# Optimization experiments

Measured on AMD Instinct MI355X. Metric: run time of the kernel, lower is better.

Reference implementation:

```python
import math
import jax, jax.numpy as jnp
import numpy as np

B, L, D_MODEL, N_HEADS = 4, 4096, 1024, 16
HEAD_DIM = D_MODEL // N_HEADS
NUM_LANDMARKS = 128


def setup_inputs() -> dict:
    key = jax.random.key(0)
    ks = jax.random.split(key, 7)
    s = 1.0 / math.sqrt(D_MODEL)
    return {
        "x": jax.random.normal(ks[0], (B, L, D_MODEL), dtype=jnp.float32),
        "Wq": jax.random.uniform(ks[1], (D_MODEL, D_MODEL), jnp.float32, -s, s),
        "bq": jax.random.uniform(ks[2], (D_MODEL,), jnp.float32, -s, s),
        "Wk": jax.random.uniform(ks[3], (D_MODEL, D_MODEL), jnp.float32, -s, s),
        "bk": jax.random.uniform(ks[4], (D_MODEL,), jnp.float32, -s, s),
        "Wv": jax.random.uniform(ks[5], (D_MODEL, D_MODEL), jnp.float32, -s, s),
        "bv": jax.random.uniform(ks[6], (D_MODEL,), jnp.float32, -s, s),
    }


def _split_heads(t):
    b, l, _ = t.shape
    return t.reshape(b, l, N_HEADS, HEAD_DIM).transpose(0, 2, 1, 3)  # [b,h,l,d]


def _iterative_inv(mat, n_iter=6):
    # Newton-Schulz pseudo-inverse on [b,h,m,m]; 'original' init uses global max.
    I = jnp.eye(mat.shape[-1], dtype=mat.dtype)
    K = mat
    V = K.swapaxes(-1, -2) / jnp.max(jnp.sum(K, axis=-2))
    for _ in range(n_iter):
        KV = jnp.matmul(K, V)
        V = jnp.matmul(0.25 * V, 13.0 * I - jnp.matmul(KV, 15.0 * I - jnp.matmul(KV, 7.0 * I - KV)))
    return V


def reference(x, Wq, bq, Wk, bk, Wv, bv):
    Q = _split_heads(x @ Wq.T + bq)
    K = _split_heads(x @ Wk.T + bk)
    V = _split_heads(x @ Wv.T + bv)
    b, h, l, d = Q.shape
    # mask is internally all-ones (module overwrites any passed mask), so the
    # -1e9*(1-mask) bias term is identically zero and mask-multiplies are no-ops.
    scale = 1.0 / math.sqrt(math.sqrt(HEAD_DIM))
    Q = Q * scale
    K = K * scale
    seg = l // NUM_LANDMARKS
    Q_lm = Q.reshape(b, h, NUM_LANDMARKS, seg, d).mean(axis=-2)  # [b,h,m,d]
    K_lm = K.reshape(b, h, NUM_LANDMARKS, seg, d).mean(axis=-2)
    kernel_1 = jax.nn.softmax(jnp.einsum('bhld,bhmd->bhlm', Q, K_lm), axis=-1)   # [b,h,l,m]
    kernel_2 = jax.nn.softmax(jnp.einsum('bhmd,bhnd->bhmn', Q_lm, K_lm), axis=-1)  # [b,h,m,m]
    kernel_3 = jax.nn.softmax(jnp.einsum('bhmd,bhld->bhml', Q_lm, K), axis=-1)   # [b,h,m,l]
    X = jnp.matmul(jnp.matmul(kernel_1, _iterative_inv(kernel_2)), jnp.matmul(kernel_3, V))  # [b,h,l,d]
    out = X.transpose(0, 2, 1, 3).reshape(b, l, h * d)
    return out
```

## Files before the change

kernel.cpp:

```cpp
#include <hip/hip_runtime.h>
#include <hip/hip_bf16.h>
#include <stdint.h>

#define DEV __device__ __forceinline__

typedef __attribute__((ext_vector_type(8))) short bf16x8;
typedef __attribute__((ext_vector_type(4))) short short4v;
typedef __attribute__((ext_vector_type(4))) float f32x4;

static constexpr int LL = 4096;
static constexpr int NH = 16;
static constexpr int HD = 64;
static constexpr int DM = 1024;
static constexpr int NL = 128;
static constexpr int BH = 64;
static constexpr int NSPLIT = 16;
static constexpr float QK_SCALE = 0.35355339059327379f;

DEV short f2bf(float f) {
  union { __hip_bfloat16 h; short s; } u;
  u.h = __float2bfloat16(f);
  return u.s;
}
DEV float bf2f(unsigned short s) {
  union { unsigned u; float f; } u;
  u.u = ((unsigned)s) << 16;
  return u.f;
}
DEV float clampf(float v) {
  return fminf(fmaxf(v, -1e6f), 1e6f);
}

DEV f32x4 mfma16(bf16x8 a, bf16x8 b, f32x4 c) {
  return __builtin_amdgcn_mfma_f32_16x16x32_bf16(a, b, c, 0, 0, 0);
}

DEV void gl2lds16(const void* g, void* l) {
  __builtin_amdgcn_global_load_lds(
      (const __attribute__((address_space(1))) void*)g,
      (__attribute__((address_space(3))) void*)l, 16, 0, 0);
}

DEV void split1(float f, short& hi, short& lo) {
  unsigned u = __float_as_uint(f);
  hi = (short)(u >> 16);
  lo = f2bf(f - __uint_as_float(u & 0xffff0000u));
}

DEV void split8(const float* av, bf16x8& hv, bf16x8& lv) {
#pragma unroll
  for (int e = 0; e < 8; e++) {
    short hi, lo;
    split1(av[e], hi, lo);
    hv[e] = hi;
    lv[e] = lo;
  }
}

__global__ __launch_bounds__(256) void cvt_kernel(
    const void* __restrict__ xv,
    const void* __restrict__ Wq, const void* __restrict__ Wk, const void* __restrict__ Wv,
    const void* __restrict__ bq, const void* __restrict__ bk, const void* __restrict__ bv,
    unsigned short* __restrict__ xb, unsigned short* __restrict__ Wb,
    float* __restrict__ bb)
{
  const int bid = blockIdx.x, t = threadIdx.x;
  __shared__ int cnt;

  auto probe_f32 = [&](const unsigned short* p) -> int {
    if (t == 0) cnt = 0;
    __syncthreads();
    int c = 0;
    for (int i = t; i < 512; i += 256) {
      unsigned e = (p[2 * i] >> 7) & 0xFF;
      if (e > 90 && e < 160) c++;
    }
    atomicAdd(&cnt, c);
    __syncthreads();
    int r = (cnt < 358);
    __syncthreads();
    return r;
  };

  auto cvt8 = [&](const void* src, unsigned short* dst, size_t i, int f32) {
    if (f32) {
      const float* s = (const float*)src + i * 8;
      f32x4 a = *(const f32x4*)s;
      f32x4 b = *(const f32x4*)(s + 4);
      bf16x8 o;
      o[0] = f2bf(a[0]); o[1] = f2bf(a[1]); o[2] = f2bf(a[2]); o[3] = f2bf(a[3]);
      o[4] = f2bf(b[0]); o[5] = f2bf(b[1]); o[6] = f2bf(b[2]); o[7] = f2bf(b[3]);
      *(bf16x8*)(dst + i * 8) = o;
    } else {
      *(bf16x8*)(dst + i * 8) =
          *(const bf16x8*)((const unsigned short*)src + i * 8);
    }
  };

  if (bid < 1536) {
    const int q = bid / 512;
    const void* src = (q == 0) ? Wq : ((q == 1) ? Wk : Wv);
    const int f32 = probe_f32((const unsigned short*)src);
    const size_t i = (size_t)(bid % 512) * 256 + t;
    cvt8(src, Wb + (size_t)q * DM * DM, i, f32);
  } else if (bid == 1536) {
    for (int q = 0; q < 3; q++) {
      const void* src = (q == 0) ? bq : ((q == 1) ? bk : bv);
      const int f32 = probe_f32((const unsigned short*)src);
      for (int i = t; i < DM; i += 256)
        bb[q * DM + i] = f32 ? ((const float*)src)[i]
                             : bf2f(((const unsigned short*)src)[i]);
      __syncthreads();
    }
  } else {
    const int xi = bid - 1537;
    const int f32 = probe_f32((const unsigned short*)xv);
#pragma unroll
    for (int k = 0; k < 4; k++) {
      const size_t i = (size_t)xi * 1024 + k * 256 + t;
      cvt8(xv, xb, i, f32);
    }
  }
}

__global__ __launch_bounds__(256, 2) void proj_kernel(
    const unsigned short* __restrict__ xb,
    const unsigned short* __restrict__ Wb,
    const float* __restrict__ bb,
    unsigned short* __restrict__ Qo, unsigned short* __restrict__ Ko,
    unsigned short* __restrict__ Vo,
    float* __restrict__ Qlm, float* __restrict__ Klm,
    unsigned short* __restrict__ Qlmb, unsigned short* __restrict__ Klmb)
{
  __shared__ __align__(16) short As[2][128 * 32];
  __shared__ __align__(16) short Bs[2][128 * 32];

  const int t = threadIdx.x;
  const int w = t >> 6;
  const int l = t & 63;
  const int lane16 = l & 15, lgrp = l >> 4;

  const int bid = blockIdx.x;
  const int mt = bid & 127;
  const int nt = bid >> 7;
  const int which = nt >> 3;
  const int m0 = mt * 128;
  const int ncol0 = (nt & 7) * 128;

  unsigned short* outp = (which == 0) ? Qo : ((which == 1) ? Ko : Vo);
  const float scl = (which == 2) ? 1.0f : QK_SCALE;

  const int srow = w * 16 + (l >> 2);
  const int skc = (l & 3) * 8;
  const unsigned short* gA = xb + (size_t)(m0 + srow) * DM + skc;
  const unsigned short* gB = Wb + (size_t)which * DM * DM + (size_t)(ncol0 + srow) * DM + skc;
  short* lA0 = As[0] + w * 512;
  short* lA1 = As[1] + w * 512;
  short* lB0 = Bs[0] + w * 512;
  short* lB1 = Bs[1] + w * 512;

  const int wm = (w >> 1) * 64;
  const int wn = (w & 1) * 64;

  f32x4 acc[4][4];
#pragma unroll
  for (int i = 0; i < 4; i++)
#pragma unroll
    for (int j = 0; j < 4; j++) acc[i][j] = f32x4{0.f, 0.f, 0.f, 0.f};

  for (int kk = 0; kk < DM; kk += 64) {
    gl2lds16(gA + kk, lA0);
    gl2lds16(gA + kk + 64 * DM, lA0 + 2048);
    gl2lds16(gA + kk + 32, lA1);
    gl2lds16(gA + kk + 32 + 64 * DM, lA1 + 2048);
    gl2lds16(gB + kk, lB0);
    gl2lds16(gB + kk + 64 * DM, lB0 + 2048);
    gl2lds16(gB + kk + 32, lB1);
    gl2lds16(gB + kk + 32 + 64 * DM, lB1 + 2048);
    __syncthreads();
#pragma unroll
    for (int kc = 0; kc < 2; kc++) {
      bf16x8 af[4], bfv[4];
#pragma unroll
      for (int i = 0; i < 4; i++) {
        af[i]  = *(const bf16x8*)&As[kc][(wm + i * 16 + lane16) * 32 + lgrp * 8];
        bfv[i] = *(const bf16x8*)&Bs[kc][(wn + i * 16 + lane16) * 32 + lgrp * 8];
      }
#pragma unroll
      for (int i = 0; i < 4; i++)
#pragma unroll
        for (int j = 0; j < 4; j++)
          acc[i][j] = mfma16(af[i], bfv[j], acc[i][j]);
    }
    __syncthreads();
  }

  const int b = m0 >> 12;
  const int hh = (ncol0 + wn) >> 6;
  float bv4[4];
#pragma unroll
  for (int j = 0; j < 4; j++)
    bv4[j] = bb[which * DM + ncol0 + wn + j * 16 + lane16];

  float seg[2][4];
#pragma unroll
  for (int s = 0; s < 2; s++)
#pragma unroll
    for (int j = 0; j < 4; j++) seg[s][j] = 0.f;

#pragma unroll
  for (int i = 0; i < 4; i++) {
#pragma unroll
    for (int j = 0; j < 4; j++) {
#pragma unroll
      for (int r = 0; r < 4; r++) {
        float v = (acc[i][j][r] + bv4[j]) * scl;
        int row = wm + i * 16 + lgrp * 4 + r;
        int li = (m0 + row) & 4095;
        int dd = (wn + j * 16 + lane16) & 63;
        outp[(((size_t)(b * NH + hh)) * LL + li) * HD + dd] = (unsigned short)f2bf(v);
        seg[i >> 1][j] += v;
      }
    }
  }
  if (which < 2) {
    float* lmb = (which == 0) ? Qlm : Klm;
    unsigned short* lmbb = (which == 0) ? Qlmb : Klmb;
#pragma unroll
    for (int s = 0; s < 2; s++) {
#pragma unroll
      for (int j = 0; j < 4; j++) {
        float ssum = seg[s][j];
        ssum += __shfl_xor(ssum, 16, 64);
        ssum += __shfl_xor(ssum, 32, 64);
        if (lgrp == 0) {
          int m = ((m0 + wm + s * 32) & 4095) >> 5;
          int dd = (wn + j * 16 + lane16) & 63;
          float mv = clampf(ssum * (1.0f / 32.0f));
          size_t idx = (((size_t)(b * NH + hh)) * NL + m) * HD + dd;
          lmb[idx] = mv;
          lmbb[idx] = (unsigned short)f2bf(mv);
        }
      }
    }
  }
}

__global__ __launch_bounds__(256, 1) void mid_kernel(
    const unsigned short* __restrict__ Qlmb, const unsigned short* __restrict__ K,
    const unsigned short* __restrict__ V,
    float* __restrict__ op, float* __restrict__ mp, float* __restrict__ lp,
    const float* __restrict__ Qlm, const float* __restrict__ Klm,
    float* __restrict__ k2, float* __restrict__ colsum_g)
{
  constexpr int LT = 64;
  constexpr int ST = 72;
  __shared__ __align__(16) short q_s[NL * ST];
  __shared__ __align__(16) short k_s[LT * ST];
  __shared__ __align__(16) short vt_s[HD * ST];
  __shared__ __align__(16) short p_s[NL * ST];

  const int t = threadIdx.x;

  if (blockIdx.x < BH * NSPLIT) {
    const int bid = blockIdx.x;
    const int bh = bid >> 4;
    const int sp = bid & (NSPLIT - 1);
    const int w = t >> 6, l = t & 63;
    const int lane16 = l & 15, lgrp = l >> 4;
    const int wm = w * 32;
    const unsigned short* Kp = K + (size_t)bh * LL * HD;
    const unsigned short* Vp = V + (size_t)bh * LL * HD;

    for (int i = t; i < NL * HD / 4; i += 256) {
      int flat = i * 4, rr = flat >> 6, dd = flat & 63;
      *(uint2*)&q_s[rr * ST + dd] = *(const uint2*)&Qlmb[(size_t)bh * NL * HD + flat];
    }

    f32x4 oacc[2][4];
    float mrun[2][4], lrun[2][4];
#pragma unroll
    for (int i = 0; i < 2; i++)
#pragma unroll
      for (int j = 0; j < 4; j++) oacc[i][j] = f32x4{0.f, 0.f, 0.f, 0.f};
#pragma unroll
    for (int i = 0; i < 2; i++)
#pragma unroll
      for (int r = 0; r < 4; r++) { mrun[i][r] = -3.0e38f; lrun[i][r] = 0.f; }

    constexpr int TPS = LL / LT / NSPLIT;
    for (int lt = sp * TPS; lt < (sp + 1) * TPS; lt++) {
      const int l0 = lt * LT;
      for (int i = t; i < LT * HD / 4; i += 256) {
        int flat = i * 4, rr = flat >> 6, dd = flat & 63;
        *(uint2*)&k_s[rr * ST + dd] = *(const uint2*)&Kp[(size_t)(l0 + rr) * HD + dd];
        uint2 raw = *(const uint2*)&Vp[(size_t)(l0 + rr) * HD + dd];
        vt_s[(dd + 0) * ST + rr] = (short)(raw.x & 0xffff);
        vt_s[(dd + 1) * ST + rr] = (short)(raw.x >> 16);
        vt_s[(dd + 2) * ST + rr] = (short)(raw.y & 0xffff);
        vt_s[(dd + 3) * ST + rr] = (short)(raw.y >> 16);
      }
      __syncthreads();

      f32x4 sacc[2][4];
#pragma unroll
      for (int i = 0; i < 2; i++)
#pragma unroll
        for (int j = 0; j < 4; j++) sacc[i][j] = f32x4{0.f, 0.f, 0.f, 0.f};
#pragma unroll
      for (int kc = 0; kc < 2; kc++) {
        bf16x8 aq[2];
#pragma unroll
        for (int i = 0; i < 2; i++)
          aq[i] = *(const bf16x8*)&q_s[(wm + i * 16 + lane16) * ST + kc * 32 + lgrp * 8];
#pragma unroll
        for (int j = 0; j < 4; j++) {
          bf16x8 bk = *(const bf16x8*)&k_s[(j * 16 + lane16) * ST + kc * 32 + lgrp * 8];
#pragma unroll
          for (int i = 0; i < 2; i++) sacc[i][j] = mfma16(aq[i], bk, sacc[i][j]);
        }
      }

#pragma unroll
      for (int i = 0; i < 2; i++) {
#pragma unroll
        for (int r = 0; r < 4; r++) {
          float tm = fmaxf(fmaxf(sacc[i][0][r], sacc[i][1][r]),
                           fmaxf(sacc[i][2][r], sacc[i][3][r]));
          tm = fmaxf(tm, __shfl_xor(tm, 1, 16));
          tm = fmaxf(tm, __shfl_xor(tm, 2, 16));
          tm = fmaxf(tm, __shfl_xor(tm, 4, 16));
          tm = fmaxf(tm, __shfl_xor(tm, 8, 16));
          float mnew = fmaxf(mrun[i][r], tm);
          float al = __expf(mrun[i][r] - mnew);
          float rs = 0.f;
#pragma unroll
          for (int j = 0; j < 4; j++) {
            float e = __expf(sacc[i][j][r] - mnew);
            sacc[i][j][r] = e;
            rs += e;
          }
          rs += __shfl_xor(rs, 1, 16);
          rs += __shfl_xor(rs, 2, 16);
          rs += __shfl_xor(rs, 4, 16);
          rs += __shfl_xor(rs, 8, 16);
          lrun[i][r] = lrun[i][r] * al + rs;
          mrun[i][r] = mnew;
#pragma unroll
          for (int j = 0; j < 4; j++) oacc[i][j][r] *= al;
          int row = wm + i * 16 + lgrp * 4 + r;
#pragma unroll
          for (int j = 0; j < 4; j++)
            p_s[row * ST + j * 16 + lane16] = f2bf(sacc[i][j][r]);
        }
      }
      __syncthreads();

#pragma unroll
      for (int kc = 0; kc < 2; kc++) {
        bf16x8 ap[2];
#pragma unroll
        for (int i = 0; i < 2; i++)
          ap[i] = *(const bf16x8*)&p_s[(wm + i * 16 + lane16) * ST + kc * 32 + lgrp * 8];
#pragma unroll
        for (int j = 0; j < 4; j++) {
          bf16x8 bv = *(const bf16x8*)&vt_s[(j * 16 + lane16) * ST + kc * 32 + lgrp * 8];
#pragma unroll
          for (int i = 0; i < 2; i++) oacc[i][j] = mfma16(ap[i], bv, oacc[i][j]);
        }
      }
      __syncthreads();
    }

    float* opp = op + ((size_t)(bh * NSPLIT + sp)) * NL * HD;
#pragma unroll
    for (int i = 0; i < 2; i++)
#pragma unroll
      for (int j = 0; j < 4; j++)
#pragma unroll
        for (int r = 0; r < 4; r++) {
          int row = wm + i * 16 + lgrp * 4 + r;
          int dd = j * 16 + lane16;
          opp[(size_t)row * HD + dd] = oacc[i][j][r];
        }
    if (lane16 == 0) {
      const size_t base = (size_t)(bh * NSPLIT + sp) * NL;
#pragma unroll
      for (int i = 0; i < 2; i++)
#pragma unroll
        for (int r = 0; r < 4; r++) {
          int row = wm + i * 16 + lgrp * 4 + r;
          mp[base + row] = mrun[i][r];
          lp[base + row] = lrun[i][r];
        }
    }
  } else {
    float* cs = (float*)q_s;
    const int bid = blockIdx.x - BH * NSPLIT;
    const int bh = bid >> 3;
    const int rc = bid & 7;
    const int r = t >> 4;
    const int c = t & 15;
    const int row = rc * 16 + r;
    const float* Q = Qlm + ((size_t)bh * NL + row) * HD;
    const float* Kf = Klm + (size_t)bh * NL * HD;
    float* k2p = k2 + (size_t)bh * NL * NL;

    for (int i = t; i < NL; i += 256) cs[i] = 0.f;

    f32x4 q4[16];
#pragma unroll
    for (int d = 0; d < 16; d++) q4[d] = *(const f32x4*)&Q[d * 4];

    float dots[8];
#pragma unroll
    for (int g = 0; g < 8; g++) {
      const float* kr = Kf + (size_t)(c + g * 16) * HD;
      float s = 0.f;
#pragma unroll
      for (int d = 0; d < 16; d++) {
        f32x4 k4 = *(const f32x4*)&kr[d * 4];
        s += q4[d][0] * k4[0];
        s += q4[d][1] * k4[1];
        s += q4[d][2] * k4[2];
        s += q4[d][3] * k4[3];
      }
      dots[g] = s;
    }

    float mx = dots[0];
#pragma unroll
    for (int g = 1; g < 8; g++) mx = fmaxf(mx, dots[g]);
    mx = fmaxf(mx, __shfl_xor(mx, 1, 16));
    mx = fmaxf(mx, __shfl_xor(mx, 2, 16));
    mx = fmaxf(mx, __shfl_xor(mx, 4, 16));
    mx = fmaxf(mx, __shfl_xor(mx, 8, 16));

    float sum = 0.f;
#pragma unroll
    for (int g = 0; g < 8; g++) {
      float e = __expf(dots[g] - mx);
      dots[g] = e;
      sum += e;
    }
    sum += __shfl_xor(sum, 1, 16);
    sum += __shfl_xor(sum, 2, 16);
    sum += __shfl_xor(sum, 4, 16);
    sum += __shfl_xor(sum, 8, 16);
    const float inv = 1.0f / fmaxf(sum, 1e-30f);

    __syncthreads();
#pragma unroll
    for (int g = 0; g < 8; g++) {
      float p = dots[g] * inv;
      k2p[(size_t)row * NL + c + g * 16] = p;
      atomicAdd(&cs[c + g * 16], p);
    }
    __syncthreads();
    for (int i = t; i < NL; i += 256) atomicAdd(&colsum_g[bh * NL + i], cs[i]);
  }
}

__global__ __launch_bounds__(256) void k3v_combine(
    const float* __restrict__ op, const float* __restrict__ mp,
    const float* __restrict__ lp, float* __restrict__ k3v)
{
  const int idx = blockIdx.x * 256 + threadIdx.x;
  const int dd = idx & 63;
  const int row = (idx >> 6) & 127;
  const int bh = idx >> 13;
  (void)dd;
  float m = -3.0e38f;
  float ms[NSPLIT];
#pragma unroll
  for (int s = 0; s < NSPLIT; s++) {
    ms[s] = mp[(size_t)(bh * NSPLIT + s) * NL + row];
    m = fmaxf(m, ms[s]);
  }
  float o = 0.f, ltot = 0.f;
#pragma unroll
  for (int s = 0; s < NSPLIT; s++) {
    float sc = __expf(ms[s] - m);
    ltot += lp[(size_t)(bh * NSPLIT + s) * NL + row] * sc;
    o += op[((size_t)(bh * NSPLIT + s) * NL + row) * HD + dd] * sc;
  }
  k3v[idx] = clampf(o / fmaxf(ltot, 1e-30f));
}

__global__ __launch_bounds__(512, 1) void ns_kernel(
    const float* __restrict__ k2, const float* __restrict__ colsum_g,
    const float* __restrict__ k3v, unsigned short* __restrict__ w2t)
{
  constexpr int VST = 132;
  constexpr int BST = 136;
  __shared__ __align__(16) float Vf[NL * VST];
  __shared__ __align__(16) short Bth[NL * BST];
  __shared__ __align__(16) short Btl[NL * BST];
  __shared__ float wmx[8];
  __shared__ float amax_s;

  const int bh = blockIdx.x, t = threadIdx.x;
  const int w = t >> 6, l = t & 63;
  const int lane16 = l & 15, lgrp = l >> 4;
  const float* K2 = k2 + (size_t)bh * NL * NL;

  float am = 0.f;
  for (int i = t; i < BH * NL; i += 512) am = fmaxf(am, colsum_g[i]);
#pragma unroll
  for (int o = 1; o < 64; o <<= 1) am = fmaxf(am, __shfl_xor(am, o, 64));
  if (l == 0) wmx[w] = am;
  __syncthreads();
  if (t == 0) {
    float m = wmx[0];
#pragma unroll
    for (int i = 1; i < 8; i++) m = fmaxf(m, wmx[i]);
    amax_s = m;
  }
  __syncthreads();
  const float inva = 1.0f / fmaxf(amax_s, 1e-30f);

  bf16x8 k2hi[4], k2lo[4];
#pragma unroll
  for (int kk = 0; kk < 4; kk++) {
    const float* ap = K2 + (size_t)(w * 16 + lane16) * NL + kk * 32 + lgrp * 8;
    f32x4 a0 = *(const f32x4*)ap;
    f32x4 a1 = *(const f32x4*)(ap + 4);
    float av[8] = {a0[0], a0[1], a0[2], a0[3], a1[0], a1[1], a1[2], a1[3]};
    split8(av, k2hi[kk], k2lo[kk]);
  }

  for (int i = t; i < NL * NL; i += 512) {
    int rr = i >> 7, cc = i & 127;
    float v = clampf(K2[(size_t)cc * NL + rr] * inva);
    Vf[rr * VST + cc] = v;
    short hi, lo; split1(v, hi, lo);
    Bth[cc * BST + rr] = hi;
    Btl[cc * BST + rr] = lo;
  }
  __syncthreads();

  f32x4 macc[8], vacc[8];

  auto mmA = [&](const bf16x8* ahi, const bf16x8* alo) {
#pragma unroll
    for (int j = 0; j < 8; j++) macc[j] = f32x4{0.f, 0.f, 0.f, 0.f};
#pragma unroll
    for (int kk = 0; kk < 4; kk++) {
#pragma unroll
      for (int j = 0; j < 8; j++) {
        const int bo = (j * 16 + lane16) * BST + kk * 32 + lgrp * 8;
        bf16x8 bh_ = *(const bf16x8*)&Bth[bo];
        bf16x8 bl_ = *(const bf16x8*)&Btl[bo];
        macc[j] = mfma16(alo[kk], bh_, macc[j]);
        macc[j] = mfma16(ahi[kk], bl_, macc[j]);
        macc[j] = mfma16(ahi[kk], bh_, macc[j]);
      }
    }
  };

  auto mmV = [&]() {
    bf16x8 ahi[4], alo[4];
#pragma unroll
    for (int kk = 0; kk < 4; kk++) {
      const float* ap = &Vf[(w * 16 + lane16) * VST + kk * 32 + lgrp * 8];
      f32x4 a0 = *(const f32x4*)ap;
      f32x4 a1 = *(const f32x4*)(ap + 4);
      float av[8] = {a0[0], a0[1], a0[2], a0[3], a1[0], a1[1], a1[2], a1[3]};
      split8(av, ahi[kk], alo[kk]);
    }
    mmA(ahi, alo);
  };

  auto writeBt = [&]() {
#pragma unroll
    for (int j = 0; j < 8; j++) {
      short4v hv, lv;
#pragma unroll
      for (int r = 0; r < 4; r++) {
        float c = clampf(macc[j][r]);
        short hi, lo; split1(c, hi, lo);
        hv[r] = hi; lv[r] = lo;
      }
      const int base = (j * 16 + lane16) * BST + w * 16 + lgrp * 4;
      *(short4v*)&Bth[base] = hv;
      *(short4v*)&Btl[base] = lv;
    }
  };

  for (int it = 0; it < 6; it++) {
    mmA(k2hi, k2lo);
    __syncthreads();
    writeBt();
    __syncthreads();

    mmV();
#pragma unroll
    for (int j = 0; j < 8; j++)
#pragma unroll
      for (int r = 0; r < 4; r++)
        vacc[j][r] = 3.25f * Vf[(w * 16 + lgrp * 4 + r) * VST + j * 16 + lane16]
                   - 3.75f * macc[j][r];
    __syncthreads();
#pragma unroll
    for (int j = 0; j < 8; j++)
#pragma unroll
      for (int r = 0; r < 4; r++)
        Vf[(w * 16 + lgrp * 4 + r) * VST + j * 16 + lane16] = clampf(macc[j][r]);
    __syncthreads();

    mmV();
#pragma unroll
    for (int j = 0; j < 8; j++)
#pragma unroll
      for (int r = 0; r < 4; r++) vacc[j][r] += 1.75f * macc[j][r];
    __syncthreads();
#pragma unroll
    for (int j = 0; j < 8; j++)
#pragma unroll
      for (int r = 0; r < 4; r++)
        Vf[(w * 16 + lgrp * 4 + r) * VST + j * 16 + lane16] = clampf(macc[j][r]);
    __syncthreads();

    mmV();
    __syncthreads();
#pragma unroll
    for (int j = 0; j < 8; j++) {
      short4v hv, lv;
#pragma unroll
      for (int r = 0; r < 4; r++) {
        float v = clampf(vacc[j][r] - 0.25f * macc[j][r]);
        Vf[(w * 16 + lgrp * 4 + r) * VST + j * 16 + lane16] = v;
        short hi, lo; split1(v, hi, lo);
        hv[r] = hi; lv[r] = lo;
      }
      const int base = (j * 16 + lane16) * BST + w * 16 + lgrp * 4;
      *(short4v*)&Bth[base] = hv;
      *(short4v*)&Btl[base] = lv;
    }
    __syncthreads();
  }

  const float* kvp = k3v + (size_t)bh * NL * HD;
  for (int i = t; i < NL * HD; i += 512) {
    int rr = i >> 6, dd = i & 63;
    float f = kvp[i];
    short hi, lo; split1(f, hi, lo);
    Bth[dd * BST + rr] = hi;
    Btl[dd * BST + rr] = lo;
  }
  __syncthreads();

  const int wr = (w & 3);
  const int wc = (w >> 2);
  f32x4 oacc[4];
#pragma unroll
  for (int j = 0; j < 4; j++) oacc[j] = f32x4{0.f, 0.f, 0.f, 0.f};
#pragma unroll
  for (int kk = 0; kk < 4; kk++) {
    const int ao = (wr * 16 + lane16) * BST + kk * 32 + lgrp * 8;
    bf16x8 ahi = *(const bf16x8*)&Bth[ao];
    bf16x8 alo = *(const bf16x8*)&Btl[ao];
#pragma unroll
    for (int j = 0; j < 4; j++) {
      const float* bp = &Vf[((wc * 4 + j) * 16 + lane16) * VST + kk * 32 + lgrp * 8];
      f32x4 b0 = *(const f32x4*)bp;
      f32x4 b1 = *(const f32x4*)(bp + 4);
      float bvv[8] = {b0[0], b0[1], b0[2], b0[3], b1[0], b1[1], b1[2], b1[3]};
      bf16x8 bhv, blv;
      split8(bvv, bhv, blv);
      oacc[j] = mfma16(alo, bhv, oacc[j]);
      oacc[j] = mfma16(ahi, blv, oacc[j]);
      oacc[j] = mfma16(ahi, bhv, oacc[j]);
    }
  }
  unsigned short* outp = w2t + (size_t)bh * HD * NL;
#pragma unroll
  for (int j = 0; j < 4; j++)
#pragma unroll
    for (int r = 0; r < 4; r++) {
      int dd = wr * 16 + lgrp * 4 + r;
      int m  = (wc * 4 + j) * 16 + lane16;
      outp[(size_t)dd * NL + m] = (unsigned short)f2bf(clampf(oacc[j][r]));
    }
}

__global__ __launch_bounds__(256, 2) void final_kernel(
    const unsigned short* __restrict__ Q, const unsigned short* __restrict__ Klmb,
    const unsigned short* __restrict__ w2t, float* __restrict__ outp)
{
  constexpr int KSD = 72;
  constexpr int PSD = 136;
  __shared__ __align__(16) short klm_s[NL * KSD];
  __shared__ __align__(16) short p_s[NL * PSD];

  const int bid = blockIdx.x;
  const int bh = bid >> 5, lt = bid & 31;
  const int l0 = lt * NL;
  const int t = threadIdx.x, w = t >> 6, l = t & 63;
  const int lane16 = l & 15, lgrp = l >> 4;
  const int wm = w * 32;
  const unsigned short* Qp = Q + (size_t)bh * LL * HD;
  const unsigned short* Kp = Klmb + (size_t)bh * NL * HD;
  const unsigned short* Wp = w2t + (size_t)bh * HD * NL;

  for (int i = t; i < NL * HD / 4; i += 256) {
    int flat = i * 4, rr = flat >> 6, dd = flat & 63;
    *(uint2*)&klm_s[rr * KSD + dd] = *(const uint2*)&Kp[flat];
  }
  __syncthreads();

  f32x4 sacc[2][8];
#pragma unroll
  for (int i = 0; i < 2; i++)
#pragma unroll
    for (int j = 0; j < 8; j++) sacc[i][j] = f32x4{0.f, 0.f, 0.f, 0.f};
#pragma unroll
  for (int kc = 0; kc < 2; kc++) {
    bf16x8 aq[2];
#pragma unroll
    for (int i = 0; i < 2; i++)
      aq[i] = *(const bf16x8*)&Qp[(size_t)(l0 + wm + i * 16 + lane16) * HD + kc * 32 + lgrp * 8];
#pragma unroll
    for (int j = 0; j < 8; j++) {
      bf16x8 bk = *(const bf16x8*)&klm_s[(j * 16 + lane16) * KSD + kc * 32 + lgrp * 8];
#pragma unroll
      for (int i = 0; i < 2; i++) sacc[i][j] = mfma16(aq[i], bk, sacc[i][j]);
    }
  }

#pragma unroll
  for (int i = 0; i < 2; i++) {
#pragma unroll
    for (int r = 0; r < 4; r++) {
      float mx = -1e30f;
#pragma unroll
      for (int j = 0; j < 8; j++) mx = fmaxf(mx, sacc[i][j][r]);
      mx = fmaxf(mx, __shfl_xor(mx, 1, 16));
      mx = fmaxf(mx, __shfl_xor(mx, 2, 16));
      mx = fmaxf(mx, __shfl_xor(mx, 4, 16));
      mx = fmaxf(mx, __shfl_xor(mx, 8, 16));
      float sum = 0.f;
#pragma unroll
      for (int j = 0; j < 8; j++) {
        float e = __expf(sacc[i][j][r] - mx);
        sacc[i][j][r] = e;
        sum += e;
      }
      sum += __shfl_xor(sum, 1, 16);
      sum += __shfl_xor(sum, 2, 16);
      sum += __shfl_xor(sum, 4, 16);
      sum += __shfl_xor(sum, 8, 16);
      float inv = 1.0f / fmaxf(sum, 1e-30f);
      int row = wm + i * 16 + lgrp * 4 + r;
#pragma unroll
      for (int j = 0; j < 8; j++)
        p_s[row * PSD + j * 16 + lane16] = f2bf(sacc[i][j][r] * inv);
    }
  }
  __syncthreads();

  f32x4 oacc[2][4];
#pragma unroll
  for (int i = 0; i < 2; i++)
#pragma unroll
    for (int j = 0; j < 4; j++) oacc[i][j] = f32x4{0.f, 0.f, 0.f, 0.f};
#pragma unroll
  for (int kc = 0; kc < 4; kc++) {
    bf16x8 ap[2];
#pragma unroll
    for (int i = 0; i < 2; i++)
      ap[i] = *(const bf16x8*)&p_s[(wm + i * 16 + lane16) * PSD + kc * 32 + lgrp * 8];
#pragma unroll
    for (int j = 0; j < 4; j++) {
      bf16x8 bw = *(const bf16x8*)&Wp[(size_t)(j * 16 + lane16) * NL + kc * 32 + lgrp * 8];
#pragma unroll
      for (int i = 0; i < 2; i++) oacc[i][j] = mfma16(ap[i], bw, oacc[i][j]);
    }
  }

  const int b = bh >> 4, h = bh & 15;
#pragma unroll
  for (int i = 0; i < 2; i++)
#pragma unroll
    for (int j = 0; j < 4; j++)
#pragma unroll
      for (int r = 0; r < 4; r++) {
        int row = wm + i * 16 + lgrp * 4 + r;
        int dd = j * 16 + lane16;
        outp[((size_t)b * LL + l0 + row) * DM + h * HD + dd] = oacc[i][j][r];
      }
}

extern "C" void kernel_launch(void* const* d_in, const int* in_sizes, int n_in,
                              void* d_out, int out_size, void* d_ws, size_t ws_size,
                              hipStream_t stream) {
  (void)in_sizes; (void)n_in; (void)out_size; (void)ws_size;
  float* outp = (float*)d_out;

  char* ws = (char*)d_ws;
  size_t off = 0;
  auto alloc = [&](size_t bytes) -> void* {
    void* p = ws + off;
    off += (bytes + 255) & ~(size_t)255;
    return p;
  };
  float* colsum_g = (float*)alloc((size_t)BH * NL * 4);
  float* Qlm = (float*)alloc((size_t)BH * NL * HD * 4);
  float* Klm = (float*)alloc((size_t)BH * NL * HD * 4);
  unsigned short* Qlmb = (unsigned short*)alloc((size_t)BH * NL * HD * 2);
  unsigned short* Klmb = (unsigned short*)alloc((size_t)BH * NL * HD * 2);
  float* k2 = (float*)alloc((size_t)BH * NL * NL * 4);
  float* k3v = (float*)alloc((size_t)BH * NL * HD * 4);
  unsigned short* w2t = (unsigned short*)alloc((size_t)BH * HD * NL * 2);
  unsigned short* Wb = (unsigned short*)alloc((size_t)3 * DM * DM * 2);
  float* bb = (float*)alloc((size_t)3 * DM * 4);
  const size_t OP_BYTES = (size_t)BH * NSPLIT * NL * HD * 4;
  const size_t ML_BYTES = (size_t)BH * NSPLIT * NL * 4;
  const size_t XB_BYTES = (size_t)4 * LL * DM * 2;
  const size_t UB_BYTES = OP_BYTES + 2 * ML_BYTES + 512;
  char* ub = (char*)alloc(UB_BYTES > XB_BYTES ? UB_BYTES : XB_BYTES);
  unsigned short* xb = (unsigned short*)ub;
  float* op = (float*)ub;
  float* mp = (float*)(ub + OP_BYTES);
  float* lp = mp + (size_t)BH * NSPLIT * NL;
  const size_t QKV = (size_t)BH * LL * HD;
  unsigned short* Qb = (unsigned short*)alloc(QKV * 2);
  unsigned short* Kb = (unsigned short*)alloc(QKV * 2);
  unsigned short* Vb = (unsigned short*)alloc(QKV * 2);

  hipMemsetAsync(colsum_g, 0, (size_t)BH * NL * 4, stream);
  cvt_kernel<<<3585, 256, 0, stream>>>(
      d_in[0], d_in[1], d_in[3], d_in[5], d_in[2], d_in[4], d_in[6],
      xb, Wb, bb);
  proj_kernel<<<128 * 24, 256, 0, stream>>>(xb, Wb, bb, Qb, Kb, Vb,
                                            Qlm, Klm, Qlmb, Klmb);
  mid_kernel<<<BH * NSPLIT + BH * 8, 256, 0, stream>>>(
      Qlmb, Kb, Vb, op, mp, lp, Qlm, Klm, k2, colsum_g);
  k3v_combine<<<BH * NL * HD / 256, 256, 0, stream>>>(op, mp, lp, k3v);
  ns_kernel<<<BH, 512, 0, stream>>>(k2, colsum_g, k3v, w2t);
  final_kernel<<<BH * 32, 256, 0, stream>>>(Qb, Klmb, w2t, outp);
}
```

Measured before the change: 451.1 us.

## Overlap kernel_1 softmax with Newton-Schulz inverse by co-scheduling blocks

Moves the Q·K_lm scoring and kernel_1 softmax out of the final kernel into extra blocks of the Newton-Schulz kernel, so they run on otherwise idle CUs while the 64 inverse blocks execute. The bf16 probability matrix is written to a global buffer that reuses the scratch area, and the final kernel now only loads P and multiplies by w2t. The trade-off is an extra global write and read of the full P matrix, plus half-idle 512-thread blocks with large static LDS that limit occupancy.

Result: no change. 449.2 us (-0.4%).

```diff
diff --git a/kernel.cpp b/kernel.cpp
--- a/kernel.cpp
+++ b/kernel.cpp
@@ -487,9 +487,11 @@
   k3v[idx] = clampf(o / fmaxf(ltot, 1e-30f));
 }
 
-__global__ __launch_bounds__(512, 1) void ns_kernel(
+__global__ __launch_bounds__(512, 1) void nsf_kernel(
     const float* __restrict__ k2, const float* __restrict__ colsum_g,
-    const float* __restrict__ k3v, unsigned short* __restrict__ w2t)
+    const float* __restrict__ k3v, unsigned short* __restrict__ w2t,
+    const unsigned short* __restrict__ Qb, const unsigned short* __restrict__ Klmb,
+    unsigned short* __restrict__ Pg)
 {
   constexpr int VST = 132;
   constexpr int BST = 136;
@@ -498,6 +500,70 @@
   __shared__ __align__(16) short Btl[NL * BST];
   __shared__ float wmx[8];
   __shared__ float amax_s;
+
+  if (blockIdx.x >= BH) {
+    const int t = threadIdx.x;
+    if (t >= 256) return;
+    const int fb = blockIdx.x - BH;
+    const int bh = fb >> 5, lt = fb & 31;
+    const int l0 = lt * NL;
+    const int w = t >> 6, l = t & 63;
+    const int lane16 = l & 15, lgrp = l >> 4;
+    const int wm = w * 32;
+    const unsigned short* Qp = Qb + (size_t)bh * LL * HD;
+    const unsigned short* Kp = Klmb + (size_t)bh * NL * HD;
+    unsigned short* Pp = Pg + (size_t)bh * LL * NL;
+
+    f32x4 sacc[2][8];
+#pragma unroll
+    for (int i = 0; i < 2; i++)
+#pragma unroll
+      for (int j = 0; j < 8; j++) sacc[i][j] = f32x4{0.f, 0.f, 0.f, 0.f};
+#pragma unroll
+    for (int kc = 0; kc < 2; kc++) {
+      bf16x8 aq[2];
+#pragma unroll
+      for (int i = 0; i < 2; i++)
+        aq[i] = *(const bf16x8*)&Qp[(size_t)(l0 + wm + i * 16 + lane16) * HD + kc * 32 + lgrp * 8];
+#pragma unroll
+      for (int j = 0; j < 8; j++) {
+        bf16x8 bk = *(const bf16x8*)&Kp[(size_t)(j * 16 + lane16) * HD + kc * 32 + lgrp * 8];
+#pragma unroll
+        for (int i = 0; i < 2; i++) sacc[i][j] = mfma16(aq[i], bk, sacc[i][j]);
+      }
+    }
+
+#pragma unroll
+    for (int i = 0; i < 2; i++) {
+#pragma unroll
+      for (int r = 0; r < 4; r++) {
+        float mx = -1e30f;
+#pragma unroll
+        for (int j = 0; j < 8; j++) mx = fmaxf(mx, sacc[i][j][r]);
+        mx = fmaxf(mx, __shfl_xor(mx, 1, 16));
+        mx = fmaxf(mx, __shfl_xor(mx, 2, 16));
+        mx = fmaxf(mx, __shfl_xor(mx, 4, 16));
+        mx = fmaxf(mx, __shfl_xor(mx, 8, 16));
+        float sum = 0.f;
+#pragma unroll
+        for (int j = 0; j < 8; j++) {
+          float e = __expf(sacc[i][j][r] - mx);
+          sacc[i][j][r] = e;
+          sum += e;
+        }
+        sum += __shfl_xor(sum, 1, 16);
+        sum += __shfl_xor(sum, 2, 16);
+        sum += __shfl_xor(sum, 4, 16);
+        sum += __shfl_xor(sum, 8, 16);
+        float inv = 1.0f / fmaxf(sum, 1e-30f);
+        int row = wm + i * 16 + lgrp * 4 + r;
+#pragma unroll
+        for (int j = 0; j < 8; j++)
+          Pp[(size_t)(l0 + row) * NL + j * 16 + lane16] = (unsigned short)f2bf(sacc[i][j][r] * inv);
+      }
+    }
+    return;
+  }
 
   const int bh = blockIdx.x, t = threadIdx.x;
   const int w = t >> 6, l = t & 63;
@@ -684,13 +750,11 @@
     }
 }
 
-__global__ __launch_bounds__(256, 2) void final_kernel(
-    const unsigned short* __restrict__ Q, const unsigned short* __restrict__ Klmb,
-    const unsigned short* __restrict__ w2t, float* __restrict__ outp)
+__global__ __launch_bounds__(256, 2) void final2_kernel(
+    const unsigned short* __restrict__ Pg, const unsigned short* __restrict__ w2t,
+    float* __restrict__ outp)
 {
-  constexpr int KSD = 72;
   constexpr int PSD = 136;
-  __shared__ __align__(16) short klm_s[NL * KSD];
   __shared__ __align__(16) short p_s[NL * PSD];
 
   const int bid = blockIdx.x;
@@ -699,63 +763,12 @@
   const int t = threadIdx.x, w = t >> 6, l = t & 63;
   const int lane16 = l & 15, lgrp = l >> 4;
   const int wm = w * 32;
-  const unsigned short* Qp = Q + (size_t)bh * LL * HD;
-  const unsigned short* Kp = Klmb + (size_t)bh * NL * HD;
+  const unsigned short* Pp = Pg + (size_t)bh * LL * NL;
   const unsigned short* Wp = w2t + (size_t)bh * HD * NL;
 
-  for (int i = t; i < NL * HD / 4; i += 256) {
-    int flat = i * 4, rr = flat >> 6, dd = flat & 63;
-    *(uint2*)&klm_s[rr * KSD + dd] = *(const uint2*)&Kp[flat];
-  }
-  __syncthreads();
-
-  f32x4 sacc[2][8];
-#pragma unroll
-  for (int i = 0; i < 2; i++)
-#pragma unroll
-    for (int j = 0; j < 8; j++) sacc[i][j] = f32x4{0.f, 0.f, 0.f, 0.f};
-#pragma unroll
-  for (int kc = 0; kc < 2; kc++) {
-    bf16x8 aq[2];
-#pragma unroll
-    for (int i = 0; i < 2; i++)
-      aq[i] = *(const bf16x8*)&Qp[(size_t)(l0 + wm + i * 16 + lane16) * HD + kc * 32 + lgrp * 8];
-#pragma unroll
-    for (int j = 0; j < 8; j++) {
-      bf16x8 bk = *(const bf16x8*)&klm_s[(j * 16 + lane16) * KSD + kc * 32 + lgrp * 8];
-#pragma unroll
-      for (int i = 0; i < 2; i++) sacc[i][j] = mfma16(aq[i], bk, sacc[i][j]);
-    }
-  }
-
-#pragma unroll
-  for (int i = 0; i < 2; i++) {
-#pragma unroll
-    for (int r = 0; r < 4; r++) {
-      float mx = -1e30f;
-#pragma unroll
-      for (int j = 0; j < 8; j++) mx = fmaxf(mx, sacc[i][j][r]);
-      mx = fmaxf(mx, __shfl_xor(mx, 1, 16));
-      mx = fmaxf(mx, __shfl_xor(mx, 2, 16));
-      mx = fmaxf(mx, __shfl_xor(mx, 4, 16));
-      mx = fmaxf(mx, __shfl_xor(mx, 8, 16));
-      float sum = 0.f;
-#pragma unroll
-      for (int j = 0; j < 8; j++) {
-        float e = __expf(sacc[i][j][r] - mx);
-        sacc[i][j][r] = e;
-        sum += e;
-      }
-      sum += __shfl_xor(sum, 1, 16);
-      sum += __shfl_xor(sum, 2, 16);
-      sum += __shfl_xor(sum, 4, 16);
-      sum += __shfl_xor(sum, 8, 16);
-      float inv = 1.0f / fmaxf(sum, 1e-30f);
-      int row = wm + i * 16 + lgrp * 4 + r;
-#pragma unroll
-      for (int j = 0; j < 8; j++)
-        p_s[row * PSD + j * 16 + lane16] = f2bf(sacc[i][j][r] * inv);
-    }
+  for (int i = t; i < NL * NL / 4; i += 256) {
+    int flat = i * 4, rr = flat >> 7, dd = flat & 127;
+    *(uint2*)&p_s[rr * PSD + dd] = *(const uint2*)&Pp[(size_t)(l0 + rr) * NL + dd];
   }
   __syncthreads();
 
@@ -817,12 +830,16 @@
   const size_t OP_BYTES = (size_t)BH * NSPLIT * NL * HD * 4;
   const size_t ML_BYTES = (size_t)BH * NSPLIT * NL * 4;
   const size_t XB_BYTES = (size_t)4 * LL * DM * 2;
-  const size_t UB_BYTES = OP_BYTES + 2 * ML_BYTES + 512;
-  char* ub = (char*)alloc(UB_BYTES > XB_BYTES ? UB_BYTES : XB_BYTES);
+  const size_t P_BYTES  = (size_t)BH * LL * NL * 2;
+  size_t ubsz = OP_BYTES + 2 * ML_BYTES + 512;
+  if (XB_BYTES > ubsz) ubsz = XB_BYTES;
+  if (P_BYTES > ubsz) ubsz = P_BYTES;
+  char* ub = (char*)alloc(ubsz);
   unsigned short* xb = (unsigned short*)ub;
   float* op = (float*)ub;
   float* mp = (float*)(ub + OP_BYTES);
   float* lp = mp + (size_t)BH * NSPLIT * NL;
+  unsigned short* Pg = (unsigned short*)ub;
   const size_t QKV = (size_t)BH * LL * HD;
   unsigned short* Qb = (unsigned short*)alloc(QKV * 2);
   unsigned short* Kb = (unsigned short*)alloc(QKV * 2);
@@ -837,6 +854,7 @@
   mid_kernel<<<BH * NSPLIT + BH * 8, 256, 0, stream>>>(
       Qlmb, Kb, Vb, op, mp, lp, Qlm, Klm, k2, colsum_g);
   k3v_combine<<<BH * NL * HD / 256, 256, 0, stream>>>(op, mp, lp, k3v);
-  ns_kernel<<<BH, 512, 0, stream>>>(k2, colsum_g, k3v, w2t);
-  final_kernel<<<BH * 32, 256, 0, stream>>>(Qb, Klmb, w2t, outp);
-}
+  nsf_kernel<<<BH + BH * 32, 512, 0, stream>>>(k2, colsum_g, k3v, w2t,
+                                               Qb, Klmb, Pg);
+  final2_kernel<<<BH * 32, 256, 0, stream>>>(Pg, w2t, outp);
+}
```
